# Kernel optimization log

Measured on AMD Instinct MI355X. Metric: run time of the kernel, lower is better.

Reference implementation:

```python
import jax, jax.numpy as jnp
import numpy as np

PI = np.pi
NQ = 9  # qubits: edge 0-2, node 3-6 (center=3, neighbor0=4), anc1=7, anc2=8


def _mlp(x, W1, b1, W2, b2):
    h = jax.nn.leaky_relu(x @ W1 + b1, negative_slope=0.2)
    return h @ W2 + b2


def _ry(t):
    h = 0.5 * t
    c = jnp.cos(h).astype(jnp.complex64)
    s = jnp.sin(h).astype(jnp.complex64)
    return jnp.stack([jnp.stack([c, -s]), jnp.stack([s, c])])


def _rx(t):
    h = 0.5 * t
    c = jnp.cos(h).astype(jnp.complex64)
    s = jnp.sin(h).astype(jnp.complex64)
    return jnp.stack([jnp.stack([c, -1j * s]), jnp.stack([-1j * s, c])])


def _rz(t):
    h = (0.5 * t).astype(jnp.complex64)
    e = jnp.exp(-1j * h)
    z = jnp.zeros((), jnp.complex64)
    return jnp.stack([jnp.stack([e, z]), jnp.stack([z, jnp.conj(e)])])


def _ap1(state, U, q):
    s = jnp.moveaxis(state, q, 0)
    s = jnp.tensordot(U, s, axes=([1], [0]))
    return jnp.moveaxis(s, 0, q)


def _apc(state, U, c, t):  # controlled-U, control c, target t
    s = jnp.moveaxis(state, (c, t), (0, 1))
    s1 = jnp.tensordot(U, s[1], axes=([1], [0]))
    s = jnp.stack([s[0], s1])
    return jnp.moveaxis(s, (0, 1), (c, t))


def _cz(state, a, b):
    s = jnp.moveaxis(state, (a, b), (0, 1))
    s = s.at[1, 1].multiply(-1.0)
    return jnp.moveaxis(s, (0, 1), (a, b))


def _pqc(data, theta):
    # data: [18] per-graphlet angles, theta: [27] shared weights; returns <X_center>
    state = jnp.zeros((2,) * NQ, jnp.complex64).at[(0,) * NQ].set(1.0)
    for i in range(3):  # edge qubits: ry, rz
        state = _ap1(state, _ry(data[2 * i]), i)
        state = _ap1(state, _rz(data[2 * i + 1]), i)
    for i in range(4):  # node qubits: ry, rz
        state = _ap1(state, _ry(data[6 + 2 * i]), 3 + i)
        state = _ap1(state, _rz(data[7 + 2 * i]), 3 + i)
    state = _apc(state, _rx(data[14]), 4, 7)  # neighbor -> anc1, c-rx(phi0)
    state = _apc(state, _ry(data[15]), 0, 7)  # edge0    -> anc1, c-ry(phi1)
    state = _apc(state, _rz(data[16]), 4, 8)  # neighbor -> anc2, c-rz(phi2)
    state = _apc(state, _ry(data[17]), 0, 8)  # edge0    -> anc2, c-ry(phi3)
    for b, qs in enumerate([(0, 4, 7), (7, 4, 8), (3, 7, 8)]):  # A, B, U blocks
        th = theta[9 * b:9 * b + 9]
        for i, q in enumerate(qs):
            state = _ap1(state, _rx(th[3 * i + 0]), q)
            state = _ap1(state, _ry(th[3 * i + 1]), q)
            state = _ap1(state, _rz(th[3 * i + 2]), q)
        state = _cz(state, qs[0], qs[1])
        state = _cz(state, qs[1], qs[2])
        state = _cz(state, qs[2], qs[0])
    xs = jnp.moveaxis(jnp.moveaxis(state, 3, 0)[::-1], 0, 3)  # apply X on qubit 3
    return jnp.real(jnp.vdot(state, xs)).astype(jnp.float32)


def setup_inputs() -> dict:
    N, E, K, G = 6000, 96000, 4, 32
    rng = np.random.default_rng(0)
    src = rng.integers(0, N, E)
    dst = (src + 1 + rng.integers(0, N - 1, E)) % N  # no self loops
    pairs = np.stack([np.minimum(src, dst), np.maximum(src, dst)], 1)
    keymap = {(int(u), int(v)): i for i, (u, v) in enumerate(pairs)}
    und = np.unique(np.concatenate([np.stack([src, dst], 1), np.stack([dst, src], 1)], 0), axis=0)
    deg = np.bincount(und[:, 0], minlength=N)
    starts = np.concatenate([[0], np.cumsum(deg)])[:-1]
    gn = np.full((N, K), -1, np.int32)
    gn[:, 0] = np.arange(N)
    ge = np.full((N, K - 1), -1, np.int32)
    for j in range(K - 1):
        has = deg > j
        cs = np.nonzero(has)[0]
        nb = und[starts[has] + j, 1]
        gn[cs, 1 + j] = nb
        for c, n in zip(cs.tolist(), nb.tolist()):
            ge[c, j] = keymap[(min(c, n), max(c, n))]
    batch = ((np.arange(N) * G) // N).astype(np.int32)
    key = jax.random.key(0)
    ks = jax.random.split(key, 12)

    def dense(k, i, o):
        return jax.random.normal(k, (i, o), jnp.float32) / np.sqrt(i)

    return dict(
        node_feat=jax.random.normal(ks[0], (N, 16), jnp.float32),
        edge_attr=jax.random.normal(ks[1], (E, 8), jnp.float32),
        node_W1=dense(ks[2], 16, 128), node_b1=jnp.zeros((128,), jnp.float32),
        node_W2=dense(ks[3], 128, 2), node_b2=jnp.zeros((2,), jnp.float32),
        edge_W1=dense(ks[4], 8, 128), edge_b1=jnp.zeros((128,), jnp.float32),
        edge_W2=dense(ks[5], 128, 2), edge_b2=jnp.zeros((2,), jnp.float32),
        theta=jax.random.uniform(ks[6], (1, 27), jnp.float32, -0.1, 0.1),
        upd_W1=dense(ks[7], 3, 128)[None], upd_b1=jnp.zeros((1, 128), jnp.float32),
        upd_W2=dense(ks[8], 128, 2)[None], upd_b2=jnp.zeros((1, 2), jnp.float32),
        head_W1=dense(ks[9], 2, 2), head_b1=jnp.zeros((2,), jnp.float32),
        head_W2=dense(ks[10], 2, 2), head_b2=jnp.zeros((2,), jnp.float32),
        graphlet_nodes=jnp.asarray(gn), graphlet_edges=jnp.asarray(ge),
        batch=jnp.asarray(batch), num_graphs=G,
    )


def reference(node_feat, edge_attr, node_W1, node_b1, node_W2, node_b2,
              edge_W1, edge_b1, edge_W2, edge_b2, theta,
              upd_W1, upd_b1, upd_W2, upd_b2,
              head_W1, head_b1, head_W2, head_b2,
              graphlet_nodes, graphlet_edges, batch, num_graphs):
    node_f = jnp.tanh(_mlp(node_feat, node_W1, node_b1, node_W2, node_b2)) * PI
    edge_f = jnp.tanh(_mlp(edge_attr, edge_W1, edge_b1, edge_W2, edge_b2)) * PI
    nm = (graphlet_nodes >= 0).astype(node_f.dtype)[..., None]  # pad mask
    em = (graphlet_edges >= 0).astype(edge_f.dtype)[..., None]
    gn = jnp.clip(graphlet_nodes, 0)
    ge = jnp.clip(graphlet_edges, 0)
    N = node_f.shape[0]
    e_feat = edge_f[ge] * em  # [N,3,2] fixed across hops
    for h in range(theta.shape[0]):
        n_feat = node_f[gn] * nm  # [N,4,2]
        phis = jnp.stack([n_feat[:, 1, 0], e_feat[:, 0, 0], n_feat[:, 1, 1], e_feat[:, 0, 1]], 1)
        data = jnp.concatenate([e_feat.reshape(N, 6), n_feat.reshape(N, 8), phis], 1)  # [N,18]
        exp = jax.vmap(_pqc, in_axes=(0, None))(data, theta[h])  # [N]
        upd_inp = jnp.concatenate([node_f[gn[:, 0]], exp[:, None]], 1)  # [N,3]
        upd = _mlp(upd_inp, upd_W1[h], upd_b1[h], upd_W2[h], upd_b2[h])  # [N,2]
        node_f = node_f + jnp.zeros_like(node_f).at[gn[:, 0]].add(upd)
    seg = jax.ops.segment_sum(node_f, batch, num_segments=num_graphs)
    cnt = jax.ops.segment_sum(jnp.ones((N,), node_f.dtype), batch, num_segments=num_graphs)
    emb = seg / cnt[:, None]  # global mean pool
    return _mlp(emb, head_W1, head_b1, head_W2, head_b2)
```

## Files before the change

kernel.cpp:

```cpp
#include <hip/hip_runtime.h>

#define PI_F 3.14159265358979323846f

struct C2 { float r, i; };
struct M2 { C2 m[2][2]; };

__device__ __forceinline__ C2 cmul(C2 a, C2 b){ return C2{a.r*b.r - a.i*b.i, a.r*b.i + a.i*b.r}; }
__device__ __forceinline__ C2 cadd(C2 a, C2 b){ return C2{a.r+b.r, a.i+b.i}; }

__device__ __forceinline__ M2 mmul(M2 A, M2 B){
  M2 R;
  #pragma unroll
  for (int r=0;r<2;++r)
    #pragma unroll
    for (int c=0;c<2;++c)
      R.m[r][c] = cadd(cmul(A.m[r][0],B.m[0][c]), cmul(A.m[r][1],B.m[1][c]));
  return R;
}
__device__ __forceinline__ M2 m_rz(float t){ float s,c; __sincosf(0.5f*t,&s,&c);
  M2 U; U.m[0][0]=C2{c,-s}; U.m[0][1]=C2{0,0}; U.m[1][0]=C2{0,0}; U.m[1][1]=C2{c,s}; return U; }
__device__ __forceinline__ M2 m_ry(float t){ float s,c; __sincosf(0.5f*t,&s,&c);
  M2 U; U.m[0][0]=C2{c,0}; U.m[0][1]=C2{-s,0}; U.m[1][0]=C2{s,0}; U.m[1][1]=C2{c,0}; return U; }
__device__ __forceinline__ M2 m_rx(float t){ float s,c; __sincosf(0.5f*t,&s,&c);
  M2 U; U.m[0][0]=C2{c,0}; U.m[0][1]=C2{0,-s}; U.m[1][0]=C2{0,-s}; U.m[1][1]=C2{c,0}; return U; }
__device__ __forceinline__ M2 fuse_zyx(float tz, float ty, float tx){ return mmul(m_rz(tz), mmul(m_ry(ty), m_rx(tx))); }

__device__ __forceinline__ float fast_tanh(float x){
  float e = __expf(2.f*x);
  return 1.f - 2.f/(e + 1.f);
}

__device__ __forceinline__ M2 loadM(const float* __restrict__ p){
  M2 U;
  U.m[0][0]=C2{p[0],p[1]}; U.m[0][1]=C2{p[2],p[3]};
  U.m[1][0]=C2{p[4],p[5]}; U.m[1][1]=C2{p[6],p[7]};
  return U;
}


template<int T>
__device__ __forceinline__ void applyT8(M2 U, float (&sr)[8], float (&si)[8]){
  #pragma unroll
  for (int a0=0;a0<8;++a0){
    if (a0 & T) continue;
    const int a1 = a0 | T;
    C2 x0{sr[a0], si[a0]}, x1{sr[a1], si[a1]};
    C2 n0 = cadd(cmul(U.m[0][0],x0), cmul(U.m[0][1],x1));
    C2 n1 = cadd(cmul(U.m[1][0],x0), cmul(U.m[1][1],x1));
    sr[a0]=n0.r; si[a0]=n0.i; sr[a1]=n1.r; si[a1]=n1.i;
  }
}

template<int XORMASK>
__device__ __forceinline__ void applySplit(M2 U, int p, float (&sr)[8], float (&si)[8]){
  const float u0r = p ? U.m[1][0].r : U.m[0][0].r;
  const float u0i = p ? U.m[1][0].i : U.m[0][0].i;
  const float u1r = p ? U.m[1][1].r : U.m[0][1].r;
  const float u1i = p ? U.m[1][1].i : U.m[0][1].i;
  #pragma unroll
  for (int a=0;a<8;++a){
    const float orr = __shfl_xor(sr[a], XORMASK);
    const float oii = __shfl_xor(si[a], XORMASK);
    const float xar = p ? orr   : sr[a], xai = p ? oii   : si[a];
    const float xbr = p ? sr[a] : orr,   xbi = p ? si[a] : oii;
    sr[a] = u0r*xar - u0i*xai + u1r*xbr - u1i*xbi;
    si[a] = u0r*xai + u0i*xar + u1r*xbi + u1i*xbr;
  }
}

template<int BA,int BB,int BC>
__device__ __forceinline__ void czTriple8(float (&sr)[8], float (&si)[8]){
  #pragma unroll
  for (int a=0;a<8;++a){
    const int x=(a&BA)?1:0, y=(a&BB)?1:0, z=(a&BC)?1:0;
    if (((x&y)^(y&z)^(z&x)) != 0){ sr[a]=-sr[a]; si[a]=-si[a]; }
  }
}

template<int BY,int BZ>
__device__ __forceinline__ void czSplit(int p, float (&sr)[8], float (&si)[8]){
  const float sg = p ? -1.f : 1.f;
  #pragma unroll
  for (int a=0;a<8;++a){
    const int y=(a&BY)?1:0, z=(a&BZ)?1:0;
    if (y & z)      { sr[a]=-sr[a];  si[a]=-si[a]; }
    else if (y | z) { sr[a]*=sg;     si[a]*=sg;    }
  }
}

__global__ void features_kernel(const float* __restrict__ node_feat,
                                const float* __restrict__ edge_attr,
                                const int* __restrict__ ge,
                                const float* __restrict__ nW1, const float* __restrict__ nb1,
                                const float* __restrict__ nW2, const float* __restrict__ nb2,
                                const float* __restrict__ eW1, const float* __restrict__ eb1,
                                const float* __restrict__ eW2, const float* __restrict__ eb2,
                                float* __restrict__ node_f, float* __restrict__ ef,
                                int N,
                                const float* __restrict__ theta, float* __restrict__ tm){
  const int t = blockIdx.x*blockDim.x + threadIdx.x;
  const int row = t >> 2;
  const int q   = t & 3;
  if (t < 9){
    M2 U = fuse_zyx(theta[3*t+2], theta[3*t+1], theta[3*t+0]);
    float* p = tm + t*8;
    p[0]=U.m[0][0].r; p[1]=U.m[0][0].i;
    p[2]=U.m[0][1].r; p[3]=U.m[0][1].i;
    p[4]=U.m[1][0].r; p[5]=U.m[1][0].i;
    p[6]=U.m[1][1].r; p[7]=U.m[1][1].i;
  }
  if (row < N){
    const float4* nf4 = reinterpret_cast<const float4*>(node_feat + (size_t)row*16);
    const float4 A = nf4[0], B = nf4[1], C = nf4[2], D = nf4[3];
    const float xi[16] = {A.x,A.y,A.z,A.w, B.x,B.y,B.z,B.w,
                          C.x,C.y,C.z,C.w, D.x,D.y,D.z,D.w};
    float a0 = 0.f, a1 = 0.f;
    #pragma unroll 4
    for (int jj=0;jj<32;++jj){
      const int j = 4*jj + q;
      float h = nb1[j];
      #pragma unroll
      for (int i=0;i<16;++i) h = fmaf(xi[i], nW1[i*128+j], h);
      h = h > 0.f ? h : 0.2f*h;
      a0 = fmaf(h, nW2[j*2+0], a0);
      a1 = fmaf(h, nW2[j*2+1], a1);
    }
    a0 += __shfl_xor(a0,1); a0 += __shfl_xor(a0,2);
    a1 += __shfl_xor(a1,1); a1 += __shfl_xor(a1,2);
    if (q == 0){
      *reinterpret_cast<float2*>(node_f + (size_t)row*2) =
          float2{PI_F * fast_tanh(nb2[0] + a0), PI_F * fast_tanh(nb2[1] + a1)};
    }
  } else {
    const int r = row - N;
    if (r >= N) return;
    const int e = ge[r*3+0];
    if (e < 0){ if (q == 0){ ef[r*2+0] = 0.f; ef[r*2+1] = 0.f; } return; }
    const float4* ea4 = reinterpret_cast<const float4*>(edge_attr + (size_t)e*8);
    const float4 A = ea4[0], B = ea4[1];
    const float xi[8] = {A.x,A.y,A.z,A.w, B.x,B.y,B.z,B.w};
    float a0 = 0.f, a1 = 0.f;
    #pragma unroll 4
    for (int jj=0;jj<32;++jj){
      const int j = 4*jj + q;
      float h = eb1[j];
      #pragma unroll
      for (int i=0;i<8;++i) h = fmaf(xi[i], eW1[i*128+j], h);
      h = h > 0.f ? h : 0.2f*h;
      a0 = fmaf(h, eW2[j*2+0], a0);
      a1 = fmaf(h, eW2[j*2+1], a1);
    }
    a0 += __shfl_xor(a0,1); a0 += __shfl_xor(a0,2);
    a1 += __shfl_xor(a1,1); a1 += __shfl_xor(a1,2);
    if (q == 0){
      *reinterpret_cast<float2*>(ef + (size_t)r*2) =
          float2{PI_F * fast_tanh(eb2[0] + a0), PI_F * fast_tanh(eb2[1] + a1)};
    }
  }
}

__global__ void __launch_bounds__(64, 1)
pqc_kernel(const float* __restrict__ node_f, const float* __restrict__ ef,
           const int* __restrict__ gn,
           const float* __restrict__ tm,
           const float* __restrict__ uW1, const float* __restrict__ ub1,
           const float* __restrict__ uW2, const float* __restrict__ ub2,
           float* __restrict__ upd, int N){
  const int t  = blockIdx.x*64 + threadIdx.x;
  const int n  = t >> 2;
  const int p0 = t & 1;
  const int p1 = (t >> 1) & 1;
  if (n >= N) return;

  const float e0 = ef[n*2+0], e1 = ef[n*2+1];
  const float f0 = node_f[n*2+0], f1 = node_f[n*2+1];
  const int v1 = gn[n*4+1];
  const bool ok = v1 >= 0; const int idx = ok ? v1 : 0;
  const float g0 = ok ? node_f[idx*2+0] : 0.f;
  const float g1 = ok ? node_f[idx*2+1] : 0.f;

  float sy0,cy0,sz0,cz0, sy3,cy3,sz3,cz3, sy4,cy4,sz4,cz4;
  __sincosf(0.5f*e0,&sy0,&cy0); __sincosf(0.5f*e1,&sz0,&cz0);
  __sincosf(0.5f*f0,&sy3,&cy3); __sincosf(0.5f*f1,&sz3,&cz3);
  __sincosf(0.5f*g0,&sy4,&cy4); __sincosf(0.5f*g1,&sz4,&cz4);

  const C2 v0[2] = { C2{cy0*cz0, -cy0*sz0}, C2{sy0*cz0, sy0*sz0} };
  const C2 v3[2] = { C2{cy3*cz3, -cy3*sz3}, C2{sy3*cz3, sy3*sz3} };
  const C2 v4[2] = { C2{cy4*cz4, -cy4*sz4}, C2{sy4*cz4, sy4*sz4} };
  const C2 vv = cmul(p0 ? v0[1] : v0[0], p1 ? v3[1] : v3[0]);

  float sr[8], si[8];
  #pragma unroll
  for (int a=0;a<8;++a){ sr[a]=0.f; si[a]=0.f; }
  #pragma unroll
  for (int b2=0;b2<2;++b2){
    const C2 a = cmul(vv, v4[b2]);
    sr[b2*4]=a.r; si[b2*4]=a.i;
  }

  #pragma unroll
  for (int a0=0;a0<8;++a0){
    if ((a0 & 2) || !(a0 & 4)) continue;
    const int a1 = a0 | 2;
    const float r0=sr[a0], i0=si[a0], r1=sr[a1], i1=si[a1];
    sr[a0] = cy4*r0 + sy4*i1;  si[a0] = cy4*i0 - sy4*r1;
    sr[a1] = sy4*i0 + cy4*r1;  si[a1] = -sy4*r0 + cy4*i1;
  }
  {
    const float sA = p0 ? sy0 : 0.f, cA = p0 ? cy0 : 1.f;
    #pragma unroll
    for (int a0=0;a0<8;++a0){
      if (a0 & 2) continue;
      const int a1 = a0 | 2;
      const float r0=sr[a0], i0=si[a0], r1=sr[a1], i1=si[a1];
      sr[a0] = cA*r0 - sA*r1;  si[a0] = cA*i0 - sA*i1;
      sr[a1] = sA*r0 + cA*r1;  si[a1] = sA*i0 + cA*i1;
    }
  }
  #pragma unroll
  for (int a=0;a<8;++a){
    if (!(a & 4)) continue;
    const float r=sr[a], im=si[a];
    if (a & 1){ sr[a] = r*cz4 - im*sz4;  si[a] = im*cz4 + r*sz4; }
    else      { sr[a] = r*cz4 + im*sz4;  si[a] = im*cz4 - r*sz4; }
  }
  {
    const float sB = p0 ? sz0 : 0.f, cB = p0 ? cz0 : 1.f;
    #pragma unroll
    for (int a0=0;a0<8;++a0){
      if (a0 & 1) continue;
      const int a1 = a0 | 1;
      const float r0=sr[a0], i0=si[a0], r1=sr[a1], i1=si[a1];
      sr[a0] = cB*r0 - sB*r1;  si[a0] = cB*i0 - sB*i1;
      sr[a1] = sB*r0 + cB*r1;  si[a1] = sB*i0 + cB*i1;
    }
  }

  applySplit<1>(loadM(tm+0*8), p0, sr, si);
  applyT8<4>(loadM(tm+1*8), sr, si);
  applyT8<2>(loadM(tm+2*8), sr, si);
  czSplit<4,2>(p0, sr, si);
  applyT8<2>(loadM(tm+3*8), sr, si);
  applyT8<4>(loadM(tm+4*8), sr, si);
  applyT8<1>(loadM(tm+5*8), sr, si);
  czTriple8<2,4,1>(sr, si);
  applySplit<2>(loadM(tm+6*8), p1, sr, si);
  applyT8<2>(loadM(tm+7*8), sr, si);
  applyT8<1>(loadM(tm+8*8), sr, si);
  czSplit<2,1>(p1, sr, si);

  float acc = 0.f;
  #pragma unroll
  for (int a=0;a<8;++a){
    const float pr = __shfl_xor(sr[a], 2);
    const float pi = __shfl_xor(si[a], 2);
    acc += sr[a]*pr + si[a]*pi;
  }
  acc += __shfl_xor(acc, 1);
  acc += __shfl_xor(acc, 2);

  const int q = t & 3;
  float o0 = 0.f, o1 = 0.f;
  #pragma unroll 4
  for (int jj=0;jj<32;++jj){
    const int j = 4*jj + q;
    float h = ub1[j];
    h = fmaf(f0,  uW1[0*128+j], h);
    h = fmaf(f1,  uW1[1*128+j], h);
    h = fmaf(acc, uW1[2*128+j], h);
    h = h > 0.f ? h : 0.2f*h;
    o0 = fmaf(h, uW2[j*2+0], o0);
    o1 = fmaf(h, uW2[j*2+1], o1);
  }
  o0 += __shfl_xor(o0, 1); o0 += __shfl_xor(o0, 2);
  o1 += __shfl_xor(o1, 1); o1 += __shfl_xor(o1, 2);
  if (q == 0){
    *reinterpret_cast<float2*>(upd + (size_t)n*2) =
        float2{f0 + ub2[0] + o0, f1 + ub2[1] + o1};
  }
}

__global__ void reduce_head_kernel(const float* __restrict__ upd,
                                   const float* __restrict__ hW1, const float* __restrict__ hb1,
                                   const float* __restrict__ hW2, const float* __restrict__ hb2,
                                   float* __restrict__ out, int N, int G){
  const int g = blockIdx.x;
  const int start = (g*N + G - 1)/G;
  const int end   = ((g+1)*N + G - 1)/G;
  float a0=0.f, a1=0.f;
  for (int n = start + threadIdx.x; n < end; n += 64){
    const float2 u = *reinterpret_cast<const float2*>(upd + (size_t)n*2);
    a0 += u.x;
    a1 += u.y;
  }
  #pragma unroll
  for (int m=32; m; m>>=1){ a0 += __shfl_xor(a0, m); a1 += __shfl_xor(a1, m); }
  if (threadIdx.x == 0){
    const float inv = 1.f / (float)(end - start);
    const float e0 = a0*inv, e1 = a1*inv;
    float h0 = hb1[0] + e0*hW1[0*2+0] + e1*hW1[1*2+0];
    float h1 = hb1[1] + e0*hW1[0*2+1] + e1*hW1[1*2+1];
    h0 = h0 > 0.f ? h0 : 0.2f*h0;
    h1 = h1 > 0.f ? h1 : 0.2f*h1;
    out[g*2+0] = hb2[0] + h0*hW2[0*2+0] + h1*hW2[1*2+0];
    out[g*2+1] = hb2[1] + h0*hW2[0*2+1] + h1*hW2[1*2+1];
  }
}

extern "C" void kernel_launch(void* const* d_in, const int* in_sizes, int n_in,
                              void* d_out, int out_size, void* d_ws, size_t ws_size,
                              hipStream_t stream) {
  const float* node_feat = (const float*)d_in[0];
  const float* edge_attr = (const float*)d_in[1];
  const float* nW1 = (const float*)d_in[2];
  const float* nb1 = (const float*)d_in[3];
  const float* nW2 = (const float*)d_in[4];
  const float* nb2 = (const float*)d_in[5];
  const float* eW1 = (const float*)d_in[6];
  const float* eb1 = (const float*)d_in[7];
  const float* eW2 = (const float*)d_in[8];
  const float* eb2 = (const float*)d_in[9];
  const float* theta = (const float*)d_in[10];
  const float* uW1 = (const float*)d_in[11];
  const float* ub1 = (const float*)d_in[12];
  const float* uW2 = (const float*)d_in[13];
  const float* ub2 = (const float*)d_in[14];
  const float* hW1 = (const float*)d_in[15];
  const float* hb1 = (const float*)d_in[16];
  const float* hW2 = (const float*)d_in[17];
  const float* hb2 = (const float*)d_in[18];
  const int* gn    = (const int*)d_in[19];
  const int* ge    = (const int*)d_in[20];

  const int N = in_sizes[0] / 16;
  const int G = out_size / 2;

  float* node_f = (float*)d_ws;
  float* ef     = node_f + (size_t)N*2;
  float* upd    = ef + (size_t)N*2;
  float* tm     = upd + (size_t)N*2;

  const int FT = 4*(2*N);
  features_kernel<<<(FT+255)/256, 256, 0, stream>>>(node_feat, edge_attr, ge,
                                                    nW1, nb1, nW2, nb2,
                                                    eW1, eb1, eW2, eb2,
                                                    node_f, ef, N, theta, tm);
  pqc_kernel<<<(4*N+63)/64, 64, 0, stream>>>(node_f, ef, gn, tm,
                                             uW1, ub1, uW2, ub2, upd, N);
  reduce_head_kernel<<<G, 64, 0, stream>>>(upd,
                                           hW1, hb1, hW2, hb2, (float*)d_out, N, G);
}
```

Baseline: 115.0 us.

## Split quantum state across 8 lanes per graphlet and vectorize feature MLPs

The PQC kernel now spreads each graphlet's reduced state vector over 8 lanes instead of 4, with 4 amplitudes per lane. Qubit 2 becomes a lane bit, so its gates go through shuffle-based split application and the CZ sign logic is rewritten for the new split. The feature MLP kernels also use 8 threads per row, each handling a contiguous 16-wide slice of hidden units with float4 weight loads. This cuts per-thread register and serial work and raises parallelism, at the cost of more shuffles and twice as many threads.

```diff
diff --git a/kernel.cpp b/kernel.cpp
--- a/kernel.cpp
+++ b/kernel.cpp
@@ -39,9 +39,9 @@
 
 
 template<int T>
-__device__ __forceinline__ void applyT8(M2 U, float (&sr)[8], float (&si)[8]){
-  #pragma unroll
-  for (int a0=0;a0<8;++a0){
+__device__ __forceinline__ void applyT4(M2 U, float (&sr)[4], float (&si)[4]){
+  #pragma unroll
+  for (int a0=0;a0<4;++a0){
     if (a0 & T) continue;
     const int a1 = a0 | T;
     C2 x0{sr[a0], si[a0]}, x1{sr[a1], si[a1]};
@@ -52,39 +52,19 @@
 }
 
 template<int XORMASK>
-__device__ __forceinline__ void applySplit(M2 U, int p, float (&sr)[8], float (&si)[8]){
+__device__ __forceinline__ void applySplit4(M2 U, int p, float (&sr)[4], float (&si)[4]){
   const float u0r = p ? U.m[1][0].r : U.m[0][0].r;
   const float u0i = p ? U.m[1][0].i : U.m[0][0].i;
   const float u1r = p ? U.m[1][1].r : U.m[0][1].r;
   const float u1i = p ? U.m[1][1].i : U.m[0][1].i;
   #pragma unroll
-  for (int a=0;a<8;++a){
+  for (int a=0;a<4;++a){
     const float orr = __shfl_xor(sr[a], XORMASK);
     const float oii = __shfl_xor(si[a], XORMASK);
     const float xar = p ? orr   : sr[a], xai = p ? oii   : si[a];
     const float xbr = p ? sr[a] : orr,   xbi = p ? si[a] : oii;
     sr[a] = u0r*xar - u0i*xai + u1r*xbr - u1i*xbi;
     si[a] = u0r*xai + u0i*xar + u1r*xbi + u1i*xbr;
-  }
-}
-
-template<int BA,int BB,int BC>
-__device__ __forceinline__ void czTriple8(float (&sr)[8], float (&si)[8]){
-  #pragma unroll
-  for (int a=0;a<8;++a){
-    const int x=(a&BA)?1:0, y=(a&BB)?1:0, z=(a&BC)?1:0;
-    if (((x&y)^(y&z)^(z&x)) != 0){ sr[a]=-sr[a]; si[a]=-si[a]; }
-  }
-}
-
-template<int BY,int BZ>
-__device__ __forceinline__ void czSplit(int p, float (&sr)[8], float (&si)[8]){
-  const float sg = p ? -1.f : 1.f;
-  #pragma unroll
-  for (int a=0;a<8;++a){
-    const int y=(a&BY)?1:0, z=(a&BZ)?1:0;
-    if (y & z)      { sr[a]=-sr[a];  si[a]=-si[a]; }
-    else if (y | z) { sr[a]*=sg;     si[a]*=sg;    }
   }
 }
 
@@ -99,8 +79,8 @@
                                 int N,
                                 const float* __restrict__ theta, float* __restrict__ tm){
   const int t = blockIdx.x*blockDim.x + threadIdx.x;
-  const int row = t >> 2;
-  const int q   = t & 3;
+  const int row = t >> 3;
+  const int q   = t & 7;
   if (t < 9){
     M2 U = fuse_zyx(theta[3*t+2], theta[3*t+1], theta[3*t+0]);
     float* p = tm + t*8;
@@ -109,24 +89,42 @@
     p[4]=U.m[1][0].r; p[5]=U.m[1][0].i;
     p[6]=U.m[1][1].r; p[7]=U.m[1][1].i;
   }
+  float h[16];
+  float a0 = 0.f, a1 = 0.f;
   if (row < N){
     const float4* nf4 = reinterpret_cast<const float4*>(node_feat + (size_t)row*16);
     const float4 A = nf4[0], B = nf4[1], C = nf4[2], D = nf4[3];
     const float xi[16] = {A.x,A.y,A.z,A.w, B.x,B.y,B.z,B.w,
                           C.x,C.y,C.z,C.w, D.x,D.y,D.z,D.w};
-    float a0 = 0.f, a1 = 0.f;
-    #pragma unroll 4
-    for (int jj=0;jj<32;++jj){
-      const int j = 4*jj + q;
-      float h = nb1[j];
+    const float4* b1v = reinterpret_cast<const float4*>(nb1 + 16*q);
+    #pragma unroll
+    for (int k=0;k<4;++k){
+      const float4 b = b1v[k];
+      h[4*k+0]=b.x; h[4*k+1]=b.y; h[4*k+2]=b.z; h[4*k+3]=b.w;
+    }
+    #pragma unroll
+    for (int i=0;i<16;++i){
+      const float4* w = reinterpret_cast<const float4*>(nW1 + i*128 + 16*q);
       #pragma unroll
-      for (int i=0;i<16;++i) h = fmaf(xi[i], nW1[i*128+j], h);
-      h = h > 0.f ? h : 0.2f*h;
-      a0 = fmaf(h, nW2[j*2+0], a0);
-      a1 = fmaf(h, nW2[j*2+1], a1);
-    }
-    a0 += __shfl_xor(a0,1); a0 += __shfl_xor(a0,2);
-    a1 += __shfl_xor(a1,1); a1 += __shfl_xor(a1,2);
+      for (int k=0;k<4;++k){
+        const float4 wv = w[k];
+        h[4*k+0] = fmaf(xi[i], wv.x, h[4*k+0]);
+        h[4*k+1] = fmaf(xi[i], wv.y, h[4*k+1]);
+        h[4*k+2] = fmaf(xi[i], wv.z, h[4*k+2]);
+        h[4*k+3] = fmaf(xi[i], wv.w, h[4*k+3]);
+      }
+    }
+    const float2* w2 = reinterpret_cast<const float2*>(nW2 + 2*(16*q));
+    #pragma unroll
+    for (int jj=0;jj<16;++jj){
+      float hv = h[jj];
+      hv = hv > 0.f ? hv : 0.2f*hv;
+      const float2 wv = w2[jj];
+      a0 = fmaf(hv, wv.x, a0);
+      a1 = fmaf(hv, wv.y, a1);
+    }
+    a0 += __shfl_xor(a0,1); a0 += __shfl_xor(a0,2); a0 += __shfl_xor(a0,4);
+    a1 += __shfl_xor(a1,1); a1 += __shfl_xor(a1,2); a1 += __shfl_xor(a1,4);
     if (q == 0){
       *reinterpret_cast<float2*>(node_f + (size_t)row*2) =
           float2{PI_F * fast_tanh(nb2[0] + a0), PI_F * fast_tanh(nb2[1] + a1)};
@@ -135,23 +133,39 @@
     const int r = row - N;
     if (r >= N) return;
     const int e = ge[r*3+0];
-    if (e < 0){ if (q == 0){ ef[r*2+0] = 0.f; ef[r*2+1] = 0.f; } return; }
+    if (e < 0){ if (q == 0){ *reinterpret_cast<float2*>(ef + (size_t)r*2) = float2{0.f,0.f}; } return; }
     const float4* ea4 = reinterpret_cast<const float4*>(edge_attr + (size_t)e*8);
     const float4 A = ea4[0], B = ea4[1];
     const float xi[8] = {A.x,A.y,A.z,A.w, B.x,B.y,B.z,B.w};
-    float a0 = 0.f, a1 = 0.f;
-    #pragma unroll 4
-    for (int jj=0;jj<32;++jj){
-      const int j = 4*jj + q;
-      float h = eb1[j];
+    const float4* b1v = reinterpret_cast<const float4*>(eb1 + 16*q);
+    #pragma unroll
+    for (int k=0;k<4;++k){
+      const float4 b = b1v[k];
+      h[4*k+0]=b.x; h[4*k+1]=b.y; h[4*k+2]=b.z; h[4*k+3]=b.w;
+    }
+    #pragma unroll
+    for (int i=0;i<8;++i){
+      const float4* w = reinterpret_cast<const float4*>(eW1 + i*128 + 16*q);
       #pragma unroll
-      for (int i=0;i<8;++i) h = fmaf(xi[i], eW1[i*128+j], h);
-      h = h > 0.f ? h : 0.2f*h;
-      a0 = fmaf(h, eW2[j*2+0], a0);
-      a1 = fmaf(h, eW2[j*2+1], a1);
-    }
-    a0 += __shfl_xor(a0,1); a0 += __shfl_xor(a0,2);
-    a1 += __shfl_xor(a1,1); a1 += __shfl_xor(a1,2);
+      for (int k=0;k<4;++k){
+        const float4 wv = w[k];
+        h[4*k+0] = fmaf(xi[i], wv.x, h[4*k+0]);
+        h[4*k+1] = fmaf(xi[i], wv.y, h[4*k+1]);
+        h[4*k+2] = fmaf(xi[i], wv.z, h[4*k+2]);
+        h[4*k+3] = fmaf(xi[i], wv.w, h[4*k+3]);
+      }
+    }
+    const float2* w2 = reinterpret_cast<const float2*>(eW2 + 2*(16*q));
+    #pragma unroll
+    for (int jj=0;jj<16;++jj){
+      float hv = h[jj];
+      hv = hv > 0.f ? hv : 0.2f*hv;
+      const float2 wv = w2[jj];
+      a0 = fmaf(hv, wv.x, a0);
+      a1 = fmaf(hv, wv.y, a1);
+    }
+    a0 += __shfl_xor(a0,1); a0 += __shfl_xor(a0,2); a0 += __shfl_xor(a0,4);
+    a1 += __shfl_xor(a1,1); a1 += __shfl_xor(a1,2); a1 += __shfl_xor(a1,4);
     if (q == 0){
       *reinterpret_cast<float2*>(ef + (size_t)r*2) =
           float2{PI_F * fast_tanh(eb2[0] + a0), PI_F * fast_tanh(eb2[1] + a1)};
@@ -166,10 +180,12 @@
            const float* __restrict__ uW1, const float* __restrict__ ub1,
            const float* __restrict__ uW2, const float* __restrict__ ub2,
            float* __restrict__ upd, int N){
-  const int t  = blockIdx.x*64 + threadIdx.x;
-  const int n  = t >> 2;
-  const int p0 = t & 1;
-  const int p1 = (t >> 1) & 1;
+  const int t   = blockIdx.x*64 + threadIdx.x;
+  const int n   = t >> 3;
+  const int sub = t & 7;
+  const int p0 = sub & 1;
+  const int p1 = (sub >> 1) & 1;
+  const int p2 = (sub >> 2) & 1;
   if (n >= N) return;
 
   const float e0 = ef[n*2+0], e1 = ef[n*2+1];
@@ -187,83 +203,102 @@
   const C2 v0[2] = { C2{cy0*cz0, -cy0*sz0}, C2{sy0*cz0, sy0*sz0} };
   const C2 v3[2] = { C2{cy3*cz3, -cy3*sz3}, C2{sy3*cz3, sy3*sz3} };
   const C2 v4[2] = { C2{cy4*cz4, -cy4*sz4}, C2{sy4*cz4, sy4*sz4} };
-  const C2 vv = cmul(p0 ? v0[1] : v0[0], p1 ? v3[1] : v3[0]);
-
-  float sr[8], si[8];
-  #pragma unroll
-  for (int a=0;a<8;++a){ sr[a]=0.f; si[a]=0.f; }
-  #pragma unroll
-  for (int b2=0;b2<2;++b2){
-    const C2 a = cmul(vv, v4[b2]);
-    sr[b2*4]=a.r; si[b2*4]=a.i;
-  }
-
-  #pragma unroll
-  for (int a0=0;a0<8;++a0){
-    if ((a0 & 2) || !(a0 & 4)) continue;
-    const int a1 = a0 | 2;
-    const float r0=sr[a0], i0=si[a0], r1=sr[a1], i1=si[a1];
-    sr[a0] = cy4*r0 + sy4*i1;  si[a0] = cy4*i0 - sy4*r1;
-    sr[a1] = sy4*i0 + cy4*r1;  si[a1] = -sy4*r0 + cy4*i1;
-  }
-  {
-    const float sA = p0 ? sy0 : 0.f, cA = p0 ? cy0 : 1.f;
-    #pragma unroll
-    for (int a0=0;a0<8;++a0){
+  const C2 vv = cmul(cmul(p0 ? v0[1] : v0[0], p1 ? v3[1] : v3[0]),
+                     p2 ? v4[1] : v4[0]);
+
+  float sr[4] = {vv.r, 0.f, 0.f, 0.f};
+  float si[4] = {vv.i, 0.f, 0.f, 0.f};
+
+  {
+    const float s = p2 ? sy4 : 0.f, c = p2 ? cy4 : 1.f;
+    #pragma unroll
+    for (int a0=0;a0<4;++a0){
       if (a0 & 2) continue;
       const int a1 = a0 | 2;
       const float r0=sr[a0], i0=si[a0], r1=sr[a1], i1=si[a1];
-      sr[a0] = cA*r0 - sA*r1;  si[a0] = cA*i0 - sA*i1;
-      sr[a1] = sA*r0 + cA*r1;  si[a1] = sA*i0 + cA*i1;
-    }
-  }
-  #pragma unroll
-  for (int a=0;a<8;++a){
-    if (!(a & 4)) continue;
-    const float r=sr[a], im=si[a];
-    if (a & 1){ sr[a] = r*cz4 - im*sz4;  si[a] = im*cz4 + r*sz4; }
-    else      { sr[a] = r*cz4 + im*sz4;  si[a] = im*cz4 - r*sz4; }
-  }
-  {
-    const float sB = p0 ? sz0 : 0.f, cB = p0 ? cz0 : 1.f;
-    #pragma unroll
-    for (int a0=0;a0<8;++a0){
+      sr[a0] = c*r0 + s*i1;  si[a0] = c*i0 - s*r1;
+      sr[a1] = s*i0 + c*r1;  si[a1] = -s*r0 + c*i1;
+    }
+  }
+  {
+    const float s = p0 ? sy0 : 0.f, c = p0 ? cy0 : 1.f;
+    #pragma unroll
+    for (int a0=0;a0<4;++a0){
+      if (a0 & 2) continue;
+      const int a1 = a0 | 2;
+      const float r0=sr[a0], i0=si[a0], r1=sr[a1], i1=si[a1];
+      sr[a0] = c*r0 - s*r1;  si[a0] = c*i0 - s*i1;
+      sr[a1] = s*r0 + c*r1;  si[a1] = s*i0 + c*i1;
+    }
+  }
+  {
+    const float sp = p2 ? sz4 : 0.f, cp = p2 ? cz4 : 1.f;
+    #pragma unroll
+    for (int a=0;a<4;++a){
+      const float r=sr[a], im=si[a];
+      if (a & 1){ sr[a] = r*cp - im*sp;  si[a] = im*cp + r*sp; }
+      else      { sr[a] = r*cp + im*sp;  si[a] = im*cp - r*sp; }
+    }
+  }
+  {
+    const float s = p0 ? sz0 : 0.f, c = p0 ? cz0 : 1.f;
+    #pragma unroll
+    for (int a0=0;a0<4;++a0){
       if (a0 & 1) continue;
       const int a1 = a0 | 1;
       const float r0=sr[a0], i0=si[a0], r1=sr[a1], i1=si[a1];
-      sr[a0] = cB*r0 - sB*r1;  si[a0] = cB*i0 - sB*i1;
-      sr[a1] = sB*r0 + cB*r1;  si[a1] = sB*i0 + cB*i1;
-    }
-  }
-
-  applySplit<1>(loadM(tm+0*8), p0, sr, si);
-  applyT8<4>(loadM(tm+1*8), sr, si);
-  applyT8<2>(loadM(tm+2*8), sr, si);
-  czSplit<4,2>(p0, sr, si);
-  applyT8<2>(loadM(tm+3*8), sr, si);
-  applyT8<4>(loadM(tm+4*8), sr, si);
-  applyT8<1>(loadM(tm+5*8), sr, si);
-  czTriple8<2,4,1>(sr, si);
-  applySplit<2>(loadM(tm+6*8), p1, sr, si);
-  applyT8<2>(loadM(tm+7*8), sr, si);
-  applyT8<1>(loadM(tm+8*8), sr, si);
-  czSplit<2,1>(p1, sr, si);
+      sr[a0] = c*r0 - s*r1;  si[a0] = c*i0 - s*i1;
+      sr[a1] = s*r0 + c*r1;  si[a1] = s*i0 + c*i1;
+    }
+  }
+
+  applySplit4<1>(loadM(tm+0*8), p0, sr, si);
+  applySplit4<4>(loadM(tm+1*8), p2, sr, si);
+  applyT4<2>(loadM(tm+2*8), sr, si);
+  {
+    const bool both = p0 && p2, any = p0 || p2;
+    #pragma unroll
+    for (int a=0;a<4;++a){
+      const bool y = (a & 2) != 0;
+      if (both || (any && y)){ sr[a]=-sr[a]; si[a]=-si[a]; }
+    }
+  }
+  applyT4<2>(loadM(tm+3*8), sr, si);
+  applySplit4<4>(loadM(tm+4*8), p2, sr, si);
+  applyT4<1>(loadM(tm+5*8), sr, si);
+  {
+    #pragma unroll
+    for (int a=0;a<4;++a){
+      const bool y7 = (a & 2) != 0, y8 = (a & 1) != 0;
+      if ((y7 && y8) || (p2 && (y7 || y8))){ sr[a]=-sr[a]; si[a]=-si[a]; }
+    }
+  }
+  applySplit4<2>(loadM(tm+6*8), p1, sr, si);
+  applyT4<2>(loadM(tm+7*8), sr, si);
+  applyT4<1>(loadM(tm+8*8), sr, si);
+  {
+    #pragma unroll
+    for (int a=0;a<4;++a){
+      const bool y7 = (a & 2) != 0, y8 = (a & 1) != 0;
+      if ((y7 && y8) || (p1 && (y7 || y8))){ sr[a]=-sr[a]; si[a]=-si[a]; }
+    }
+  }
 
   float acc = 0.f;
   #pragma unroll
-  for (int a=0;a<8;++a){
+  for (int a=0;a<4;++a){
     const float pr = __shfl_xor(sr[a], 2);
     const float pi = __shfl_xor(si[a], 2);
     acc += sr[a]*pr + si[a]*pi;
   }
   acc += __shfl_xor(acc, 1);
   acc += __shfl_xor(acc, 2);
-
-  const int q = t & 3;
+  acc += __shfl_xor(acc, 4);
+
   float o0 = 0.f, o1 = 0.f;
   #pragma unroll 4
-  for (int jj=0;jj<32;++jj){
-    const int j = 4*jj + q;
+  for (int jj=0;jj<16;++jj){
+    const int j = 8*jj + sub;
     float h = ub1[j];
     h = fmaf(f0,  uW1[0*128+j], h);
     h = fmaf(f1,  uW1[1*128+j], h);
@@ -272,9 +307,9 @@
     o0 = fmaf(h, uW2[j*2+0], o0);
     o1 = fmaf(h, uW2[j*2+1], o1);
   }
-  o0 += __shfl_xor(o0, 1); o0 += __shfl_xor(o0, 2);
-  o1 += __shfl_xor(o1, 1); o1 += __shfl_xor(o1, 2);
-  if (q == 0){
+  o0 += __shfl_xor(o0, 1); o0 += __shfl_xor(o0, 2); o0 += __shfl_xor(o0, 4);
+  o1 += __shfl_xor(o1, 1); o1 += __shfl_xor(o1, 2); o1 += __shfl_xor(o1, 4);
+  if (sub == 0){
     *reinterpret_cast<float2*>(upd + (size_t)n*2) =
         float2{f0 + ub2[0] + o0, f1 + ub2[1] + o1};
   }
@@ -340,12 +375,12 @@
   float* upd    = ef + (size_t)N*2;
   float* tm     = upd + (size_t)N*2;
 
-  const int FT = 4*(2*N);
+  const int FT = 8*(2*N);
   features_kernel<<<(FT+255)/256, 256, 0, stream>>>(node_feat, edge_attr, ge,
                                                     nW1, nb1, nW2, nb2,
                                                     eW1, eb1, eW2, eb2,
                                                     node_f, ef, N, theta, tm);
-  pqc_kernel<<<(4*N+63)/64, 64, 0, stream>>>(node_f, ef, gn, tm,
+  pqc_kernel<<<(8*N+63)/64, 64, 0, stream>>>(node_f, ef, gn, tm,
                                              uW1, ub1, uW2, ub2, upd, N);
   reduce_head_kernel<<<G, 64, 0, stream>>>(upd,
                                            hW1, hb1, hW2, hb2, (float*)d_out, N, G);
```

After: 118.4 us. 1.03x slower.
